# Kernel tuning notes

Hardware: AMD Instinct MI355X
Metric: run time of the kernel (lower is better)

The kernel has to match this reference:

```python
import jax, jax.numpy as jnp
import numpy as np

BATCH = 2
L = 2048
D_MODEL = 1024
D_STATE = 16
D_CONV = 4
EXPAND = 2
D_INNER = EXPAND * D_MODEL  # 2048
DT_RANK = (D_MODEL + 15) // 16  # 64


def setup_inputs() -> dict:
    key = jax.random.key(0)
    ks = jax.random.split(key, 12)
    f = jnp.float32
    hidden_states = jax.random.normal(ks[0], (BATCH, L, D_MODEL), f)
    input2 = jax.random.normal(ks[1], (BATCH, L, D_MODEL), f)
    in_proj1_w = jax.random.normal(ks[2], (D_INNER, D_MODEL), f) * (D_MODEL ** -0.5)
    in_proj2_w = jax.random.normal(ks[3], (D_INNER, D_MODEL), f) * (D_MODEL ** -0.5)
    conv_w = jax.random.normal(ks[4], (D_INNER, 1, D_CONV), f) * (D_CONV ** -0.5)
    conv_b = jax.random.normal(ks[5], (D_INNER,), f) * 0.02
    x_proj_w = jax.random.normal(ks[6], (DT_RANK + 2 * D_STATE, D_INNER), f) * (D_INNER ** -0.5)
    dt_std = DT_RANK ** -0.5
    dt_proj_w = jax.random.uniform(ks[7], (D_INNER, DT_RANK), f, -dt_std, dt_std)
    # dt bias init: inverse softplus of log-uniform dt in [1e-3, 1e-1]
    dt = jnp.exp(jax.random.uniform(ks[8], (D_INNER,), f) * (np.log(0.1) - np.log(0.001)) + np.log(0.001))
    dt = jnp.clip(dt, 1e-4, None)
    dt_proj_b = dt + jnp.log(-jnp.expm1(-dt))
    # A_log init: log(1..d_state) broadcast over channels
    A_log = jnp.log(jnp.broadcast_to(jnp.arange(1, D_STATE + 1, dtype=f), (D_INNER, D_STATE)))
    D = jnp.ones((D_INNER,), f)
    out_proj_w = jax.random.normal(ks[9], (D_MODEL, D_INNER), f) * (D_INNER ** -0.5)
    return dict(hidden_states=hidden_states, input2=input2, in_proj1_w=in_proj1_w,
                in_proj2_w=in_proj2_w, conv_w=conv_w, conv_b=conv_b, x_proj_w=x_proj_w,
                dt_proj_w=dt_proj_w, dt_proj_b=dt_proj_b, A_log=A_log, D=D,
                out_proj_w=out_proj_w)


def _forward(hidden_states, input2, in_proj1_w, in_proj2_w, conv_w, conv_b,
             x_proj_w, dt_proj_w, dt_proj_b, A_log, D, out_proj_w):
    # in_proj: (B,L,Dm) -> (B,d_inner,L)
    x = jnp.einsum('bld,ed->bel', hidden_states, in_proj1_w)
    z = jnp.einsum('bld,ed->bel', input2, in_proj2_w)
    # causal depthwise conv1d (left pad d_conv-1, equiv to torch pad+truncate) + SiLU
    xc = jax.lax.conv_general_dilated(x, conv_w, (1,), [(D_CONV - 1, 0)],
                                      dimension_numbers=('NCH', 'OIH', 'NCH'),
                                      feature_group_count=D_INNER)
    x = jax.nn.silu(xc + conv_b[None, :, None])
    # x_proj -> dt, B, C
    x_dbl = jnp.einsum('bel,re->brl', x, x_proj_w)  # (B, dt_rank+2n, L)
    dt = x_dbl[:, :DT_RANK]
    Bm = x_dbl[:, DT_RANK:DT_RANK + D_STATE]       # (B, n, L)
    Cm = x_dbl[:, DT_RANK + D_STATE:]               # (B, n, L)
    delta = jnp.einsum('brl,er->bel', dt, dt_proj_w)
    delta = jax.nn.softplus(delta + dt_proj_b[None, :, None])  # (B, d_inner, L)
    A = -jnp.exp(A_log)  # (d_inner, n)
    # selective scan over time (time-major for lax.scan)
    dlt = jnp.transpose(delta, (2, 0, 1))  # (L, B, d)
    u = jnp.transpose(x, (2, 0, 1))        # (L, B, d)
    Bt = jnp.transpose(Bm, (2, 0, 1))      # (L, B, n)
    Ct = jnp.transpose(Cm, (2, 0, 1))      # (L, B, n)

    def step(state, inp):
        d_t, u_t, B_t, C_t = inp
        dA = jnp.exp(d_t[..., None] * A)                        # (B, d, n)
        state = state * dA + (d_t * u_t)[..., None] * B_t[:, None, :]
        y_t = jnp.einsum('bdn,bn->bd', state, C_t)
        return state, y_t

    init = jnp.zeros((hidden_states.shape[0], D_INNER, D_STATE), x.dtype)
    _, ys = jax.lax.scan(step, init, (dlt, u, Bt, Ct))
    y = jnp.transpose(ys, (1, 2, 0)) + D[None, :, None] * x  # (B, d, L)
    y = y * jax.nn.silu(z)
    out = jnp.einsum('bel,de->bld', y, out_proj_w)  # out_proj, no bias
    return out


def reference(hidden_states, input2, in_proj1_w, in_proj2_w, conv_w, conv_b,
              x_proj_w, dt_proj_w, dt_proj_b, A_log, D, out_proj_w):
    return _forward(hidden_states, input2, in_proj1_w, in_proj2_w, conv_w, conv_b,
                    x_proj_w, dt_proj_w, dt_proj_b, A_log, D, out_proj_w)
```

## Files before the change

### kernel.cpp

```cpp
#include <hip/hip_runtime.h>
#include <cstddef>
#include <cmath>
#include <type_traits>

#define BATCH 2
#define LSEQ 2048
#define DM 1024
#define DSTATE 16
#define DI 2048
#define DTR 64
#define XDR 96
#define NC 32
#define TC 64
#define PN (4096 * 96)

using f32x4 = __attribute__((ext_vector_type(4))) float;
using bf16x8 = __attribute__((ext_vector_type(8))) short;
typedef unsigned short ushort_t;

__device__ __forceinline__ unsigned short f2bf(float f) {
  union { float f; unsigned int u; } c; c.f = f;
  unsigned int u = c.u;
  return (unsigned short)((u + 0x7FFFu + ((u >> 16) & 1u)) >> 16);
}
__device__ __forceinline__ float bf2f(unsigned short h) {
  union { unsigned int u; float f; } c; c.u = ((unsigned int)h) << 16;
  return c.f;
}
__device__ __forceinline__ unsigned int pack2(float a, float b) {
  return (unsigned int)f2bf(a) | ((unsigned int)f2bf(b) << 16);
}

__device__ __forceinline__ void gl_lds16(const void* g, void* l) {
  __builtin_amdgcn_global_load_lds(
      (const __attribute__((address_space(1))) void*)g,
      (__attribute__((address_space(3))) void*)l, 16, 0, 0);
}

__global__ __launch_bounds__(256) void cvt_bf16_kernel(
    const float* __restrict__ s, unsigned short* __restrict__ d, int n8) {
  int i = blockIdx.x * 256 + threadIdx.x;
  if (i >= n8) return;
  const float4* sp = reinterpret_cast<const float4*>(s) + (size_t)i * 2;
  float4 a = sp[0], b = sp[1];
  uint4 v = make_uint4(pack2(a.x, a.y), pack2(a.z, a.w), pack2(b.x, b.y),
                       pack2(b.z, b.w));
  *(reinterpret_cast<uint4*>(d) + i) = v;
}

template <typename OutT>
__global__ __launch_bounds__(256) void gemm_bf16_t(
    const unsigned short* __restrict__ A, const unsigned short* __restrict__ B,
    OutT* __restrict__ C, int K, int lda, int ldb, int ldc) {
  __shared__ __align__(16) unsigned short As[128][64];
  __shared__ __align__(16) unsigned short Bs[128][64];

  const int tid = threadIdx.x;
  const int lane = tid & 63;
  const int w = tid >> 6;

  const int gx = gridDim.x;
  const int nwg = gx * gridDim.y;
  const int id = blockIdx.y * gx + blockIdx.x;
  const int cpx = nwg >> 3;
  const int lt = (id & 7) * cpx + (id >> 3);
  const size_t m0 = (size_t)(lt / gx) * 128;
  const size_t n0 = (size_t)(lt % gx) * 128;

  const int rsub = lane >> 3;
  const int sslot = (lane & 7) ^ rsub;
  const unsigned short* Ab = A + m0 * lda + (size_t)rsub * lda + sslot * 8;
  const unsigned short* Bb = B + n0 * ldb + (size_t)rsub * ldb + sslot * 8;

  f32x4 acc[4][4] = {};

  const int fr = lane & 15;
  const int q = lane >> 4;
  const int f7 = fr & 7;

  for (int k0 = 0; k0 < K; k0 += 64) {
#pragma unroll
    for (int i = 0; i < 4; ++i) {
      const int r0 = w * 32 + i * 8;
      gl_lds16(Ab + (size_t)r0 * lda + k0, &As[r0][0]);
      gl_lds16(Bb + (size_t)r0 * ldb + k0, &Bs[r0][0]);
    }
    __syncthreads();

    bf16x8 af[4][2], bf_[4][2];
#pragma unroll
    for (int i = 0; i < 4; ++i) {
#pragma unroll
      for (int kk = 0; kk < 2; ++kk) {
        const int sA = (((kk * 4 + q) ^ f7) << 3);
        af[i][kk] = *reinterpret_cast<const bf16x8*>(
            &As[(w >> 1) * 64 + i * 16 + fr][sA]);
        bf_[i][kk] = *reinterpret_cast<const bf16x8*>(
            &Bs[(w & 1) * 64 + i * 16 + fr][sA]);
      }
    }
#pragma unroll
    for (int kk = 0; kk < 2; ++kk)
#pragma unroll
      for (int i = 0; i < 4; ++i)
#pragma unroll
        for (int j = 0; j < 4; ++j)
          acc[i][j] = __builtin_amdgcn_mfma_f32_16x16x32_bf16(
              af[i][kk], bf_[j][kk], acc[i][j], 0, 0, 0);
    __syncthreads();
  }

  const int crb = q * 4;
#pragma unroll
  for (int i = 0; i < 4; ++i) {
    size_t row = m0 + (w >> 1) * 64 + i * 16 + crb;
#pragma unroll
    for (int j = 0; j < 4; ++j) {
      size_t col = n0 + (w & 1) * 64 + j * 16 + fr;
#pragma unroll
      for (int r = 0; r < 4; ++r) {
        if constexpr (std::is_same_v<OutT, unsigned short>)
          C[(row + r) * ldc + col] = f2bf(acc[i][j][r]);
        else
          C[(row + r) * ldc + col] = acc[i][j][r];
      }
    }
  }
}

__global__ __launch_bounds__(256) void gemm_xdbl(
    const unsigned short* __restrict__ A,
    const unsigned short* __restrict__ B,
    float* __restrict__ P) {
  __shared__ __align__(16) unsigned short As[128][64];
  __shared__ __align__(16) unsigned short Bs[96][64];

  const int tid = threadIdx.x;
  const int lane = tid & 63;
  const int w = tid >> 6;
  const size_t m0 = (size_t)blockIdx.x * 128;
  const int k0base = blockIdx.y * 512;

  const int rsub = lane >> 3;
  const int sslot = (lane & 7) ^ rsub;
  const unsigned short* Ab = A + m0 * DI + (size_t)rsub * DI + sslot * 8;
  const unsigned short* Bb = B + (size_t)rsub * DI + sslot * 8;

  f32x4 acc[4][3] = {};

  const int fr = lane & 15;
  const int q = lane >> 4;
  const int f7 = fr & 7;

  for (int ks = 0; ks < 8; ++ks) {
    const int k0 = k0base + ks * 64;
#pragma unroll
    for (int i = 0; i < 4; ++i) {
      const int r0 = w * 32 + i * 8;
      gl_lds16(Ab + (size_t)r0 * DI + k0, &As[r0][0]);
    }
#pragma unroll
    for (int i = 0; i < 3; ++i) {
      const int r0 = w * 24 + i * 8;
      gl_lds16(Bb + (size_t)r0 * DI + k0, &Bs[r0][0]);
    }
    __syncthreads();

    bf16x8 af[4][2], bf_[3][2];
#pragma unroll
    for (int kk = 0; kk < 2; ++kk) {
      const int sA = (((kk * 4 + q) ^ f7) << 3);
#pragma unroll
      for (int i = 0; i < 4; ++i)
        af[i][kk] = *reinterpret_cast<const bf16x8*>(
            &As[(w >> 1) * 64 + i * 16 + fr][sA]);
#pragma unroll
      for (int j = 0; j < 3; ++j)
        bf_[j][kk] = *reinterpret_cast<const bf16x8*>(
            &Bs[(w & 1) * 48 + j * 16 + fr][sA]);
    }
#pragma unroll
    for (int kk = 0; kk < 2; ++kk)
#pragma unroll
      for (int i = 0; i < 4; ++i)
#pragma unroll
        for (int j = 0; j < 3; ++j)
          acc[i][j] = __builtin_amdgcn_mfma_f32_16x16x32_bf16(
              af[i][kk], bf_[j][kk], acc[i][j], 0, 0, 0);
    __syncthreads();
  }

  float* Pz = P + (size_t)blockIdx.y * PN;
  const int crb = q * 4;
#pragma unroll
  for (int i = 0; i < 4; ++i) {
    size_t row = m0 + (w >> 1) * 64 + i * 16 + crb;
#pragma unroll
    for (int j = 0; j < 3; ++j) {
      int col = (w & 1) * 48 + j * 16 + fr;
#pragma unroll
      for (int r = 0; r < 4; ++r) Pz[(row + r) * XDR + col] = acc[i][j][r];
    }
  }
}

__global__ __launch_bounds__(256) void reduce4x_kernel(
    const float* __restrict__ P, unsigned short* __restrict__ dtB,
    float* __restrict__ BC) {
  int i = blockIdx.x * 256 + threadIdx.x;
  int row = i / XDR, col = i - row * XDR;
  float s = (P[i] + P[PN + i]) + (P[2 * PN + i] + P[3 * PN + i]);
  if (col < 64)
    dtB[row * 64 + col] = f2bf(s);
  else
    BC[row * 32 + (col - 64)] = s;
}

__global__ __launch_bounds__(256) void conv_silu_kernel(
    const float* __restrict__ x, const float* __restrict__ w,
    const float* __restrict__ cb, unsigned short* __restrict__ out) {
  int idx = blockIdx.x * 256 + threadIdx.x;
  int e4 = idx % (DI / 4);
  int bl = idx / (DI / 4);
  int l = bl % LSEQ;
  int e = e4 * 4;

  const float4* cw = reinterpret_cast<const float4*>(w);
  float4 w0 = cw[e], w1 = cw[e + 1], w2 = cw[e + 2], w3 = cw[e + 3];
  float4 acc = *reinterpret_cast<const float4*>(&cb[e]);

#define TAPK(K, COMP)                                                       \
  {                                                                         \
    int ls = l - 3 + (K);                                                   \
    if (ls >= 0) {                                                          \
      float4 xv = *reinterpret_cast<const float4*>(                         \
          &x[((size_t)(bl) - 3 + (K)) * DI + e]);                           \
      acc.x = fmaf(xv.x, w0.COMP, acc.x);                                   \
      acc.y = fmaf(xv.y, w1.COMP, acc.y);                                   \
      acc.z = fmaf(xv.z, w2.COMP, acc.z);                                   \
      acc.w = fmaf(xv.w, w3.COMP, acc.w);                                   \
    }                                                                       \
  }
  TAPK(0, x)
  TAPK(1, y)
  TAPK(2, z)
  TAPK(3, w)
#undef TAPK

  acc.x = acc.x / (1.f + expf(-acc.x));
  acc.y = acc.y / (1.f + expf(-acc.y));
  acc.z = acc.z / (1.f + expf(-acc.z));
  acc.w = acc.w / (1.f + expf(-acc.w));
  *reinterpret_cast<uint2*>(&out[(size_t)bl * DI + e]) =
      make_uint2(pack2(acc.x, acc.y), pack2(acc.z, acc.w));
}

__device__ __forceinline__ float softplus_fast(float x) {
  float ex = __expf(x);
  return (x > 20.f) ? x : __logf(1.f + ex);
}

__global__ __launch_bounds__(256) void scan_passA(
    const float* __restrict__ draw, const unsigned short* __restrict__ u,
    const float* __restrict__ bc, const float* __restrict__ dtb,
    const float* __restrict__ A_log, float* __restrict__ sEnd,
    float* __restrict__ sProd) {
  int g = blockIdx.x * 256 + threadIdx.x;
  int e = g & (DI - 1);
  int c = (g >> 11) & (NC - 1);
  int b = g >> 16;

  float nA[DSTATE];
#pragma unroll
  for (int n = 0; n < DSTATE; ++n) nA[n] = -__expf(A_log[e * DSTATE + n]);
  const float bias = dtb[e];

  size_t off = ((size_t)b * LSEQ + c * TC) * DI + e;
  size_t boff = ((size_t)b * LSEQ + c * TC) * 32;

  float s[DSTATE], P[DSTATE];
#pragma unroll
  for (int n = 0; n < DSTATE; ++n) { s[n] = 0.f; P[n] = 1.f; }

  float dr = draw[off];
  float ut = bf2f(u[off]);
  float4 B0 = *reinterpret_cast<const float4*>(&bc[boff]);
  float4 B1 = *reinterpret_cast<const float4*>(&bc[boff + 4]);
  float4 B2 = *reinterpret_cast<const float4*>(&bc[boff + 8]);
  float4 B3 = *reinterpret_cast<const float4*>(&bc[boff + 12]);

  for (int t = 0; t < TC; ++t) {
    float dr_n = 0.f, ut_n = 0.f;
    float4 B0n = {}, B1n = {}, B2n = {}, B3n = {};
    if (t + 1 < TC) {
      dr_n = draw[off + DI];
      ut_n = bf2f(u[off + DI]);
      B0n = *reinterpret_cast<const float4*>(&bc[boff + 32]);
      B1n = *reinterpret_cast<const float4*>(&bc[boff + 36]);
      B2n = *reinterpret_cast<const float4*>(&bc[boff + 40]);
      B3n = *reinterpret_cast<const float4*>(&bc[boff + 44]);
    }

    float d = softplus_fast(dr + bias);
    float db = d * ut;
    float Bv[DSTATE] = {B0.x, B0.y, B0.z, B0.w, B1.x, B1.y, B1.z, B1.w,
                        B2.x, B2.y, B2.z, B2.w, B3.x, B3.y, B3.z, B3.w};
#pragma unroll
    for (int n = 0; n < DSTATE; ++n) {
      float dA = __expf(d * nA[n]);
      s[n] = fmaf(s[n], dA, db * Bv[n]);
      P[n] *= dA;
    }
    off += DI;
    boff += 32;
    dr = dr_n; ut = ut_n;
    B0 = B0n; B1 = B1n; B2 = B2n; B3 = B3n;
  }

  size_t o = (((size_t)b * NC + c) * DI + e) * DSTATE;
  float4* se = reinterpret_cast<float4*>(&sEnd[o]);
  float4* sp = reinterpret_cast<float4*>(&sProd[o]);
  se[0] = make_float4(s[0], s[1], s[2], s[3]);
  se[1] = make_float4(s[4], s[5], s[6], s[7]);
  se[2] = make_float4(s[8], s[9], s[10], s[11]);
  se[3] = make_float4(s[12], s[13], s[14], s[15]);
  sp[0] = make_float4(P[0], P[1], P[2], P[3]);
  sp[1] = make_float4(P[4], P[5], P[6], P[7]);
  sp[2] = make_float4(P[8], P[9], P[10], P[11]);
  sp[3] = make_float4(P[12], P[13], P[14], P[15]);
}

__global__ __launch_bounds__(256) void scan_passB(
    const float* __restrict__ sEnd, const float* __restrict__ sProd,
    float* __restrict__ sInit) {
  int g = blockIdx.x * 256 + threadIdx.x;
  int n = g & 15;
  int e = (g >> 4) & (DI - 1);
  int b = g >> 15;
  float s = 0.f;
  for (int c = 0; c < NC; ++c) {
    size_t o = (((size_t)b * NC + c) * DI + e) * DSTATE + n;
    sInit[o] = s;
    s = fmaf(s, sProd[o], sEnd[o]);
  }
}

__global__ __launch_bounds__(256) void scan_passC(
    const float* __restrict__ draw, const unsigned short* __restrict__ u,
    const unsigned short* __restrict__ z, const float* __restrict__ bc,
    const float* __restrict__ dtb, const float* __restrict__ A_log,
    const float* __restrict__ Dv, const float* __restrict__ sInit,
    unsigned short* __restrict__ gOut) {
  int g = blockIdx.x * 256 + threadIdx.x;
  int e = g & (DI - 1);
  int c = (g >> 11) & (NC - 1);
  int b = g >> 16;

  float nA[DSTATE];
#pragma unroll
  for (int n = 0; n < DSTATE; ++n) nA[n] = -__expf(A_log[e * DSTATE + n]);
  const float bias = dtb[e];
  const float Dval = Dv[e];

  size_t off = ((size_t)b * LSEQ + c * TC) * DI + e;
  size_t boff = ((size_t)b * LSEQ + c * TC) * 32;

  float s[DSTATE];
  {
    size_t o = (((size_t)b * NC + c) * DI + e) * DSTATE;
    const float4* si = reinterpret_cast<const float4*>(&sInit[o]);
    float4 s0 = si[0], s1 = si[1], s2 = si[2], s3 = si[3];
    s[0] = s0.x; s[1] = s0.y; s[2] = s0.z; s[3] = s0.w;
    s[4] = s1.x; s[5] = s1.y; s[6] = s1.z; s[7] = s1.w;
    s[8] = s2.x; s[9] = s2.y; s[10] = s2.z; s[11] = s2.w;
    s[12] = s3.x; s[13] = s3.y; s[14] = s3.z; s[15] = s3.w;
  }

  float dr = draw[off];
  float ut = bf2f(u[off]);
  float zt = bf2f(z[off]);
  float4 B0 = *reinterpret_cast<const float4*>(&bc[boff]);
  float4 B1 = *reinterpret_cast<const float4*>(&bc[boff + 4]);
  float4 B2 = *reinterpret_cast<const float4*>(&bc[boff + 8]);
  float4 B3 = *reinterpret_cast<const float4*>(&bc[boff + 12]);
  float4 C0 = *reinterpret_cast<const float4*>(&bc[boff + 16]);
  float4 C1 = *reinterpret_cast<const float4*>(&bc[boff + 20]);
  float4 C2 = *reinterpret_cast<const float4*>(&bc[boff + 24]);
  float4 C3 = *reinterpret_cast<const float4*>(&bc[boff + 28]);

  for (int t = 0; t < TC; ++t) {
    float dr_n = 0.f, ut_n = 0.f, zt_n = 0.f;
    float4 B0n = {}, B1n = {}, B2n = {}, B3n = {};
    float4 C0n = {}, C1n = {}, C2n = {}, C3n = {};
    if (t + 1 < TC) {
      dr_n = draw[off + DI];
      ut_n = bf2f(u[off + DI]);
      zt_n = bf2f(z[off + DI]);
      B0n = *reinterpret_cast<const float4*>(&bc[boff + 32]);
      B1n = *reinterpret_cast<const float4*>(&bc[boff + 36]);
      B2n = *reinterpret_cast<const float4*>(&bc[boff + 40]);
      B3n = *reinterpret_cast<const float4*>(&bc[boff + 44]);
      C0n = *reinterpret_cast<const float4*>(&bc[boff + 48]);
      C1n = *reinterpret_cast<const float4*>(&bc[boff + 52]);
      C2n = *reinterpret_cast<const float4*>(&bc[boff + 56]);
      C3n = *reinterpret_cast<const float4*>(&bc[boff + 60]);
    }

    float d = softplus_fast(dr + bias);
    float db = d * ut;
    float Bv[DSTATE] = {B0.x, B0.y, B0.z, B0.w, B1.x, B1.y, B1.z, B1.w,
                        B2.x, B2.y, B2.z, B2.w, B3.x, B3.y, B3.z, B3.w};
    float Cv[DSTATE] = {C0.x, C0.y, C0.z, C0.w, C1.x, C1.y, C1.z, C1.w,
                        C2.x, C2.y, C2.z, C2.w, C3.x, C3.y, C3.z, C3.w};
    float y = 0.f;
#pragma unroll
    for (int n = 0; n < DSTATE; ++n) {
      float dA = __expf(d * nA[n]);
      s[n] = fmaf(s[n], dA, db * Bv[n]);
      y = fmaf(s[n], Cv[n], y);
    }
    float gate = zt / (1.f + __expf(-zt));
    gOut[off] = f2bf((y + Dval * ut) * gate);

    off += DI;
    boff += 32;
    dr = dr_n; ut = ut_n; zt = zt_n;
    B0 = B0n; B1 = B1n; B2 = B2n; B3 = B3n;
    C0 = C0n; C1 = C1n; C2 = C2n; C3 = C3n;
  }
}

extern "C" void kernel_launch(void* const* d_in, const int* in_sizes, int n_in,
                              void* d_out, int out_size, void* d_ws,
                              size_t ws_size, hipStream_t stream) {
  const float* hs = (const float*)d_in[0];
  const float* in2 = (const float*)d_in[1];
  const float* w1 = (const float*)d_in[2];
  const float* w2 = (const float*)d_in[3];
  const float* cw = (const float*)d_in[4];
  const float* cb = (const float*)d_in[5];
  const float* xpw = (const float*)d_in[6];
  const float* dtw = (const float*)d_in[7];
  const float* dtb = (const float*)d_in[8];
  const float* alog = (const float*)d_in[9];
  const float* Dv = (const float*)d_in[10];
  const float* ow = (const float*)d_in[11];
  float* out = (float*)d_out;

  const size_t BLE = (size_t)BATCH * LSEQ * DI;
  const size_t BLM = (size_t)BATCH * LSEQ * DM;
  const size_t WN = (size_t)DI * DM;
  const size_t SC = (size_t)BATCH * NC * DI * DSTATE;

  float* W = (float*)d_ws;
  float* bufX = W;
  float* M2 = W + BLE;
  float* M3 = M2 + BLE / 2;
  float* M4 = M3 + BLE / 2;
  float* sEnd = M4 + BLE / 2;
  float* sProd = sEnd + SC;
  float* sInit = sProd + SC;
  float* BC = sInit + SC;

  unsigned short* hsb = (unsigned short*)M2;
  unsigned short* zb = (unsigned short*)M2;
  unsigned short* in2b = (unsigned short*)M3;
  unsigned short* ub = (unsigned short*)M3;
  unsigned short* wb1 = (unsigned short*)M4;
  unsigned short* wb2 = wb1 + WN;
  float* xdblP = M4;
  unsigned short* xpwB = (unsigned short*)(M4 + 4 * PN);
  unsigned short* dtB = (unsigned short*)(M4 + 4 * PN + 98304 + 16);
  unsigned short* dtwB = (unsigned short*)(M4 + 4 * PN + 98304 + 131072 + 32);
  unsigned short* bufG = (unsigned short*)M4;
  unsigned short* owb = (unsigned short*)sInit;

  const int M = BATCH * LSEQ;
  dim3 blk(256);

  cvt_bf16_kernel<<<(int)(BLM / 8 / 256), blk, 0, stream>>>(hs, hsb,
                                                            (int)(BLM / 8));
  cvt_bf16_kernel<<<(int)(BLM / 8 / 256), blk, 0, stream>>>(in2, in2b,
                                                            (int)(BLM / 8));
  cvt_bf16_kernel<<<(int)(WN / 8 / 256), blk, 0, stream>>>(w1, wb1,
                                                           (int)(WN / 8));
  cvt_bf16_kernel<<<(int)(WN / 8 / 256), blk, 0, stream>>>(w2, wb2,
                                                           (int)(WN / 8));
  gemm_bf16_t<float><<<dim3(DI / 128, M / 128), blk, 0, stream>>>(
      hsb, wb1, bufX, DM, DM, DM, DI);
  gemm_bf16_t<unsigned short><<<dim3(DI / 128, M / 128), blk, 0, stream>>>(
      in2b, wb2, zb, DM, DM, DM, DI);
  conv_silu_kernel<<<(M * (DI / 4)) / 256, blk, 0, stream>>>(bufX, cw, cb, ub);
  cvt_bf16_kernel<<<96, blk, 0, stream>>>(xpw, xpwB, XDR * DI / 8);
  cvt_bf16_kernel<<<64, blk, 0, stream>>>(dtw, dtwB, DI * DTR / 8);
  gemm_xdbl<<<dim3(M / 128, 4), blk, 0, stream>>>(ub, xpwB, xdblP);
  reduce4x_kernel<<<(M * XDR) / 256, blk, 0, stream>>>(xdblP, dtB, BC);
  gemm_bf16_t<float><<<dim3(DI / 128, M / 128), blk, 0, stream>>>(
      dtB, dtwB, bufX, DTR, DTR, DTR, DI);
  scan_passA<<<(BATCH * DI * NC) / 256, blk, 0, stream>>>(bufX, ub, BC, dtb,
                                                          alog, sEnd, sProd);
  scan_passB<<<(BATCH * DI * DSTATE) / 256, blk, 0, stream>>>(sEnd, sProd,
                                                              sInit);
  scan_passC<<<(BATCH * DI * NC) / 256, blk, 0, stream>>>(
      bufX, ub, zb, BC, dtb, alog, Dv, sInit, bufG);
  cvt_bf16_kernel<<<(int)(WN / 8 / 256), blk, 0, stream>>>(ow, owb,
                                                           (int)(WN / 8));
  gemm_bf16_t<float><<<dim3(DM / 128, M / 128), blk, 0, stream>>>(
      bufG, owb, out, DI, DI, DI, DM);
}
```

Baseline: 256.1 us.

## Fuse softplus into delta GEMM, exploit A structure, double scan chunks

A new delta GEMM applies the bias and softplus in its epilogue and stores delta as bf16, so both scan passes stop recomputing softplus and read half the bytes. The scan passes check at runtime whether the A rows are integer multiples of the first entry; when they are, the 16 exponentials per step become one exponential followed by a chain of multiplies. The chunk count doubles (NC 64, TC 32) to give more parallelism with shorter serial loops. The prefix pass now writes in place, removing the sInit buffer. Risks are bf16 rounding of delta and error building up through the repeated-multiply powers.

```diff
diff --git a/kernel.cpp b/kernel.cpp
--- a/kernel.cpp
+++ b/kernel.cpp
@@ -10,13 +10,12 @@
 #define DI 2048
 #define DTR 64
 #define XDR 96
-#define NC 32
-#define TC 64
+#define NC 64
+#define TC 32
 #define PN (4096 * 96)
 
 using f32x4 = __attribute__((ext_vector_type(4))) float;
 using bf16x8 = __attribute__((ext_vector_type(8))) short;
-typedef unsigned short ushort_t;
 
 __device__ __forceinline__ unsigned short f2bf(float f) {
   union { float f; unsigned int u; } c; c.f = f;
@@ -35,6 +34,11 @@
   __builtin_amdgcn_global_load_lds(
       (const __attribute__((address_space(1))) void*)g,
       (__attribute__((address_space(3))) void*)l, 16, 0, 0);
+}
+
+__device__ __forceinline__ float softplus_fast(float x) {
+  float ex = __expf(x);
+  return (x > 20.f) ? x : __logf(1.f + ex);
 }
 
 __global__ __launch_bounds__(256) void cvt_bf16_kernel(
@@ -124,6 +128,83 @@
         else
           C[(row + r) * ldc + col] = acc[i][j][r];
       }
+    }
+  }
+}
+
+__global__ __launch_bounds__(256) void gemm_delta(
+    const unsigned short* __restrict__ A, const unsigned short* __restrict__ B,
+    const float* __restrict__ bias, unsigned short* __restrict__ C, int K,
+    int lda, int ldb, int ldc) {
+  __shared__ __align__(16) unsigned short As[128][64];
+  __shared__ __align__(16) unsigned short Bs[128][64];
+
+  const int tid = threadIdx.x;
+  const int lane = tid & 63;
+  const int w = tid >> 6;
+
+  const int gx = gridDim.x;
+  const int nwg = gx * gridDim.y;
+  const int id = blockIdx.y * gx + blockIdx.x;
+  const int cpx = nwg >> 3;
+  const int lt = (id & 7) * cpx + (id >> 3);
+  const size_t m0 = (size_t)(lt / gx) * 128;
+  const size_t n0 = (size_t)(lt % gx) * 128;
+
+  const int rsub = lane >> 3;
+  const int sslot = (lane & 7) ^ rsub;
+  const unsigned short* Ab = A + m0 * lda + (size_t)rsub * lda + sslot * 8;
+  const unsigned short* Bb = B + n0 * ldb + (size_t)rsub * ldb + sslot * 8;
+
+  f32x4 acc[4][4] = {};
+
+  const int fr = lane & 15;
+  const int q = lane >> 4;
+  const int f7 = fr & 7;
+
+  for (int k0 = 0; k0 < K; k0 += 64) {
+#pragma unroll
+    for (int i = 0; i < 4; ++i) {
+      const int r0 = w * 32 + i * 8;
+      gl_lds16(Ab + (size_t)r0 * lda + k0, &As[r0][0]);
+      gl_lds16(Bb + (size_t)r0 * ldb + k0, &Bs[r0][0]);
+    }
+    __syncthreads();
+
+    bf16x8 af[4][2], bf_[4][2];
+#pragma unroll
+    for (int i = 0; i < 4; ++i) {
+#pragma unroll
+      for (int kk = 0; kk < 2; ++kk) {
+        const int sA = (((kk * 4 + q) ^ f7) << 3);
+        af[i][kk] = *reinterpret_cast<const bf16x8*>(
+            &As[(w >> 1) * 64 + i * 16 + fr][sA]);
+        bf_[i][kk] = *reinterpret_cast<const bf16x8*>(
+            &Bs[(w & 1) * 64 + i * 16 + fr][sA]);
+      }
+    }
+#pragma unroll
+    for (int kk = 0; kk < 2; ++kk)
+#pragma unroll
+      for (int i = 0; i < 4; ++i)
+#pragma unroll
+        for (int j = 0; j < 4; ++j)
+          acc[i][j] = __builtin_amdgcn_mfma_f32_16x16x32_bf16(
+              af[i][kk], bf_[j][kk], acc[i][j], 0, 0, 0);
+    __syncthreads();
+  }
+
+  const int crb = q * 4;
+#pragma unroll
+  for (int i = 0; i < 4; ++i) {
+    size_t row = m0 + (w >> 1) * 64 + i * 16 + crb;
+#pragma unroll
+    for (int j = 0; j < 4; ++j) {
+      size_t col = n0 + (w & 1) * 64 + j * 16 + fr;
+      float bv = bias[col];
+#pragma unroll
+      for (int r = 0; r < 4; ++r)
+        C[(row + r) * ldc + col] = f2bf(softplus_fast(acc[i][j][r] + bv));
     }
   }
 }
@@ -255,25 +336,24 @@
       make_uint2(pack2(acc.x, acc.y), pack2(acc.z, acc.w));
 }
 
-__device__ __forceinline__ float softplus_fast(float x) {
-  float ex = __expf(x);
-  return (x > 20.f) ? x : __logf(1.f + ex);
-}
-
 __global__ __launch_bounds__(256) void scan_passA(
-    const float* __restrict__ draw, const unsigned short* __restrict__ u,
-    const float* __restrict__ bc, const float* __restrict__ dtb,
-    const float* __restrict__ A_log, float* __restrict__ sEnd,
-    float* __restrict__ sProd) {
+    const unsigned short* __restrict__ dB, const unsigned short* __restrict__ u,
+    const float* __restrict__ bc, const float* __restrict__ A_log,
+    float* __restrict__ sEnd, float* __restrict__ sProd) {
   int g = blockIdx.x * 256 + threadIdx.x;
   int e = g & (DI - 1);
   int c = (g >> 11) & (NC - 1);
-  int b = g >> 16;
+  int b = g >> 17;
 
   float nA[DSTATE];
 #pragma unroll
   for (int n = 0; n < DSTATE; ++n) nA[n] = -__expf(A_log[e * DSTATE + n]);
-  const float bias = dtb[e];
+  const float nA0 = nA[0];
+  bool aok = true;
+#pragma unroll
+  for (int n = 1; n < DSTATE; ++n)
+    aok = aok && (fabsf(nA[n] - (float)(n + 1) * nA0) <=
+                  1e-4f * fabsf(nA[n]));
 
   size_t off = ((size_t)b * LSEQ + c * TC) * DI + e;
   size_t boff = ((size_t)b * LSEQ + c * TC) * 32;
@@ -282,7 +362,7 @@
 #pragma unroll
   for (int n = 0; n < DSTATE; ++n) { s[n] = 0.f; P[n] = 1.f; }
 
-  float dr = draw[off];
+  float d = bf2f(dB[off]);
   float ut = bf2f(u[off]);
   float4 B0 = *reinterpret_cast<const float4*>(&bc[boff]);
   float4 B1 = *reinterpret_cast<const float4*>(&bc[boff + 4]);
@@ -290,10 +370,10 @@
   float4 B3 = *reinterpret_cast<const float4*>(&bc[boff + 12]);
 
   for (int t = 0; t < TC; ++t) {
-    float dr_n = 0.f, ut_n = 0.f;
+    float d_n = 0.f, ut_n = 0.f;
     float4 B0n = {}, B1n = {}, B2n = {}, B3n = {};
     if (t + 1 < TC) {
-      dr_n = draw[off + DI];
+      d_n = bf2f(dB[off + DI]);
       ut_n = bf2f(u[off + DI]);
       B0n = *reinterpret_cast<const float4*>(&bc[boff + 32]);
       B1n = *reinterpret_cast<const float4*>(&bc[boff + 36]);
@@ -301,19 +381,27 @@
       B3n = *reinterpret_cast<const float4*>(&bc[boff + 44]);
     }
 
-    float d = softplus_fast(dr + bias);
     float db = d * ut;
+    float dA[DSTATE];
+    if (aok) {
+      float qq = __expf(d * nA0);
+      dA[0] = qq;
+#pragma unroll
+      for (int n = 1; n < DSTATE; ++n) dA[n] = dA[n - 1] * qq;
+    } else {
+#pragma unroll
+      for (int n = 0; n < DSTATE; ++n) dA[n] = __expf(d * nA[n]);
+    }
     float Bv[DSTATE] = {B0.x, B0.y, B0.z, B0.w, B1.x, B1.y, B1.z, B1.w,
                         B2.x, B2.y, B2.z, B2.w, B3.x, B3.y, B3.z, B3.w};
 #pragma unroll
     for (int n = 0; n < DSTATE; ++n) {
-      float dA = __expf(d * nA[n]);
-      s[n] = fmaf(s[n], dA, db * Bv[n]);
-      P[n] *= dA;
+      s[n] = fmaf(s[n], dA[n], db * Bv[n]);
+      P[n] *= dA[n];
     }
     off += DI;
     boff += 32;
-    dr = dr_n; ut = ut_n;
+    d = d_n; ut = ut_n;
     B0 = B0n; B1 = B1n; B2 = B2n; B3 = B3n;
   }
 
@@ -331,8 +419,7 @@
 }
 
 __global__ __launch_bounds__(256) void scan_passB(
-    const float* __restrict__ sEnd, const float* __restrict__ sProd,
-    float* __restrict__ sInit) {
+    float* __restrict__ sEnd, const float* __restrict__ sProd) {
   int g = blockIdx.x * 256 + threadIdx.x;
   int n = g & 15;
   int e = (g >> 4) & (DI - 1);
@@ -340,26 +427,32 @@
   float s = 0.f;
   for (int c = 0; c < NC; ++c) {
     size_t o = (((size_t)b * NC + c) * DI + e) * DSTATE + n;
-    sInit[o] = s;
-    s = fmaf(s, sProd[o], sEnd[o]);
+    float se = sEnd[o];
+    float sp = sProd[o];
+    sEnd[o] = s;
+    s = fmaf(s, sp, se);
   }
 }
 
 __global__ __launch_bounds__(256) void scan_passC(
-    const float* __restrict__ draw, const unsigned short* __restrict__ u,
+    const unsigned short* __restrict__ dB, const unsigned short* __restrict__ u,
     const unsigned short* __restrict__ z, const float* __restrict__ bc,
-    const float* __restrict__ dtb, const float* __restrict__ A_log,
-    const float* __restrict__ Dv, const float* __restrict__ sInit,
-    unsigned short* __restrict__ gOut) {
+    const float* __restrict__ A_log, const float* __restrict__ Dv,
+    const float* __restrict__ sInit, unsigned short* __restrict__ gOut) {
   int g = blockIdx.x * 256 + threadIdx.x;
   int e = g & (DI - 1);
   int c = (g >> 11) & (NC - 1);
-  int b = g >> 16;
+  int b = g >> 17;
 
   float nA[DSTATE];
 #pragma unroll
   for (int n = 0; n < DSTATE; ++n) nA[n] = -__expf(A_log[e * DSTATE + n]);
-  const float bias = dtb[e];
+  const float nA0 = nA[0];
+  bool aok = true;
+#pragma unroll
+  for (int n = 1; n < DSTATE; ++n)
+    aok = aok && (fabsf(nA[n] - (float)(n + 1) * nA0) <=
+                  1e-4f * fabsf(nA[n]));
   const float Dval = Dv[e];
 
   size_t off = ((size_t)b * LSEQ + c * TC) * DI + e;
@@ -376,7 +469,7 @@
     s[12] = s3.x; s[13] = s3.y; s[14] = s3.z; s[15] = s3.w;
   }
 
-  float dr = draw[off];
+  float d = bf2f(dB[off]);
   float ut = bf2f(u[off]);
   float zt = bf2f(z[off]);
   float4 B0 = *reinterpret_cast<const float4*>(&bc[boff]);
@@ -389,11 +482,11 @@
   float4 C3 = *reinterpret_cast<const float4*>(&bc[boff + 28]);
 
   for (int t = 0; t < TC; ++t) {
-    float dr_n = 0.f, ut_n = 0.f, zt_n = 0.f;
+    float d_n = 0.f, ut_n = 0.f, zt_n = 0.f;
     float4 B0n = {}, B1n = {}, B2n = {}, B3n = {};
     float4 C0n = {}, C1n = {}, C2n = {}, C3n = {};
     if (t + 1 < TC) {
-      dr_n = draw[off + DI];
+      d_n = bf2f(dB[off + DI]);
       ut_n = bf2f(u[off + DI]);
       zt_n = bf2f(z[off + DI]);
       B0n = *reinterpret_cast<const float4*>(&bc[boff + 32]);
@@ -406,8 +499,17 @@
       C3n = *reinterpret_cast<const float4*>(&bc[boff + 60]);
     }
 
-    float d = softplus_fast(dr + bias);
     float db = d * ut;
+    float dA[DSTATE];
+    if (aok) {
+      float qq = __expf(d * nA0);
+      dA[0] = qq;
+#pragma unroll
+      for (int n = 1; n < DSTATE; ++n) dA[n] = dA[n - 1] * qq;
+    } else {
+#pragma unroll
+      for (int n = 0; n < DSTATE; ++n) dA[n] = __expf(d * nA[n]);
+    }
     float Bv[DSTATE] = {B0.x, B0.y, B0.z, B0.w, B1.x, B1.y, B1.z, B1.w,
                         B2.x, B2.y, B2.z, B2.w, B3.x, B3.y, B3.z, B3.w};
     float Cv[DSTATE] = {C0.x, C0.y, C0.z, C0.w, C1.x, C1.y, C1.z, C1.w,
@@ -415,8 +517,7 @@
     float y = 0.f;
 #pragma unroll
     for (int n = 0; n < DSTATE; ++n) {
-      float dA = __expf(d * nA[n]);
-      s[n] = fmaf(s[n], dA, db * Bv[n]);
+      s[n] = fmaf(s[n], dA[n], db * Bv[n]);
       y = fmaf(s[n], Cv[n], y);
     }
     float gate = zt / (1.f + __expf(-zt));
@@ -424,7 +525,7 @@
 
     off += DI;
     boff += 32;
-    dr = dr_n; ut = ut_n; zt = zt_n;
+    d = d_n; ut = ut_n; zt = zt_n;
     B0 = B0n; B1 = B1n; B2 = B2n; B3 = B3n;
     C0 = C0n; C1 = C1n; C2 = C2n; C3 = C3n;
   }
@@ -459,8 +560,7 @@
   float* M4 = M3 + BLE / 2;
   float* sEnd = M4 + BLE / 2;
   float* sProd = sEnd + SC;
-  float* sInit = sProd + SC;
-  float* BC = sInit + SC;
+  float* BC = sProd + SC;
 
   unsigned short* hsb = (unsigned short*)M2;
   unsigned short* zb = (unsigned short*)M2;
@@ -473,7 +573,8 @@
   unsigned short* dtB = (unsigned short*)(M4 + 4 * PN + 98304 + 16);
   unsigned short* dtwB = (unsigned short*)(M4 + 4 * PN + 98304 + 131072 + 32);
   unsigned short* bufG = (unsigned short*)M4;
-  unsigned short* owb = (unsigned short*)sInit;
+  unsigned short* dB = (unsigned short*)bufX;
+  unsigned short* owb = (unsigned short*)sProd;
 
   const int M = BATCH * LSEQ;
   dim3 blk(256);
@@ -495,16 +596,15 @@
   cvt_bf16_kernel<<<64, blk, 0, stream>>>(dtw, dtwB, DI * DTR / 8);
   gemm_xdbl<<<dim3(M / 128, 4), blk, 0, stream>>>(ub, xpwB, xdblP);
   reduce4x_kernel<<<(M * XDR) / 256, blk, 0, stream>>>(xdblP, dtB, BC);
-  gemm_bf16_t<float><<<dim3(DI / 128, M / 128), blk, 0, stream>>>(
-      dtB, dtwB, bufX, DTR, DTR, DTR, DI);
-  scan_passA<<<(BATCH * DI * NC) / 256, blk, 0, stream>>>(bufX, ub, BC, dtb,
-                                                          alog, sEnd, sProd);
-  scan_passB<<<(BATCH * DI * DSTATE) / 256, blk, 0, stream>>>(sEnd, sProd,
-                                                              sInit);
-  scan_passC<<<(BATCH * DI * NC) / 256, blk, 0, stream>>>(
-      bufX, ub, zb, BC, dtb, alog, Dv, sInit, bufG);
+  gemm_delta<<<dim3(DI / 128, M / 128), blk, 0, stream>>>(
+      dtB, dtwB, dtb, dB, DTR, DTR, DTR, DI);
+  scan_passA<<<(BATCH * DI * NC) / 256, blk, 0, stream>>>(dB, ub, BC, alog,
+                                                          sEnd, sProd);
+  scan_passB<<<(BATCH * DI * DSTATE) / 256, blk, 0, stream>>>(sEnd, sProd);
   cvt_bf16_kernel<<<(int)(WN / 8 / 256), blk, 0, stream>>>(ow, owb,
                                                            (int)(WN / 8));
+  scan_passC<<<(BATCH * DI * NC) / 256, blk, 0, stream>>>(
+      dB, ub, zb, BC, alog, Dv, sEnd, bufG);
   gemm_bf16_t<float><<<dim3(DM / 128, M / 128), blk, 0, stream>>>(
       bufG, owb, out, DI, DI, DI, DM);
 }
```

Measured after the change: 249.3 us. 1.03x faster.
